# Performance work log

Measured on AMD Instinct MI355X. Metric: run time of the kernel, lower is better.

Reference implementation:

```python
import jax, jax.numpy as jnp
import numpy as np

N = 8192       # paired user/item batch
D_IN = 10000   # interaction-vector length
H = 1024       # hidden width
E = 128        # shared embedding dim


def setup_inputs() -> dict:
    key = jax.random.key(0)
    ks = jax.random.split(key, 10)
    g = 5.0 / 3.0  # tanh gain used by the torch init

    def xavier(k, shape):
        fan_in, fan_out = shape
        std = g * np.sqrt(2.0 / (fan_in + fan_out))
        return jax.random.normal(k, shape, dtype=jnp.float32) * std

    return {
        "user_data": jax.random.normal(ks[0], (N, D_IN), dtype=jnp.float32),
        "item_data": jax.random.normal(ks[1], (N, D_IN), dtype=jnp.float32),
        "Wu1": xavier(ks[2], (D_IN, H)),
        "bu1": jnp.full((H,), 0.01, dtype=jnp.float32),
        "Wu2": xavier(ks[3], (H, E)),
        "bu2": jnp.full((E,), 0.01, dtype=jnp.float32),
        "Wi1": xavier(ks[4], (D_IN, H)),
        "bi1": jnp.full((H,), 0.01, dtype=jnp.float32),
        "Wi2": xavier(ks[5], (H, E)),
        "bi2": jnp.full((E,), 0.01, dtype=jnp.float32),
    }


def reference(user_data, item_data, Wu1, bu1, Wu2, bu2, Wi1, bi1, Wi2, bi2):
    # Encoders (dropout is identity at inference). PolyLinear: Linear -> ReLU -> Linear.
    p = jax.nn.relu(user_data @ Wu1 + bu1) @ Wu2 + bu2   # [N, E]
    q = jax.nn.relu(item_data @ Wi1 + bi1) @ Wi2 + bi2   # [N, E]
    # (p @ q.T).diag() == row-wise dot product; identical math, O(N*E) not O(N^2*E).
    return jnp.einsum("ne,ne->n", p, q)
```

## Files before the change

kernel.cpp:

```cpp
#include <hip/hip_runtime.h>
#include <hip/hip_bf16.h>
#include <stdint.h>

#define KP   10112
#define DIN  10000
#define NB   8192
#define HID  1024
#define EMB  128
#define NKT  313
#define NI   79

typedef __attribute__((ext_vector_type(8))) __bf16 bf16x8;
typedef __attribute__((ext_vector_type(4))) float  f32x4;
typedef __attribute__((ext_vector_type(4))) unsigned short ushort4v;

typedef const __attribute__((address_space(1))) void* gas_cp;
typedef __attribute__((address_space(3))) void* las_p;

__device__ __forceinline__ unsigned short f2bf(float f) {
    union { float f; unsigned u; } c; c.f = f;
    unsigned u = c.u;
    u += 0x7FFFu + ((u >> 16) & 1u);
    return (unsigned short)(u >> 16);
}

__global__ void conv_pad(const float* __restrict__ src, unsigned short* __restrict__ dst) {
    const int c4  = blockIdx.x * blockDim.x + threadIdx.x;
    const int row = blockIdx.y;
    if (c4 >= KP / 4) return;
    ushort4v o;
    if (c4 < DIN / 4) {
        float4 a = *(const float4*)(src + (size_t)row * DIN + (size_t)c4 * 4);
        o[0] = f2bf(a.x); o[1] = f2bf(a.y); o[2] = f2bf(a.z); o[3] = f2bf(a.w);
    } else {
        o[0] = o[1] = o[2] = o[3] = 0;
    }
    *(ushort4v*)(dst + (size_t)row * KP + (size_t)c4 * 4) = o;
}

__global__ void conv_transpose(const float* __restrict__ src, unsigned short* __restrict__ dst,
                               int K, int N, int Kp) {
    __shared__ float tile[64][33];
    const int tx = threadIdx.x & 31, ty = threadIdx.x >> 5;
    const int k0 = blockIdx.x * 64, n0 = blockIdx.y * 32;
#pragma unroll
    for (int j = 0; j < 8; ++j) {
        int k = k0 + ty + j * 8;
        tile[ty + j * 8][tx] = (k < K) ? src[(size_t)k * N + n0 + tx] : 0.0f;
    }
    __syncthreads();
#pragma unroll
    for (int j = 0; j < 4; ++j) {
        int n = n0 + ty + j * 8;
        unsigned short lo = f2bf(tile[2 * tx][ty + j * 8]);
        unsigned short hi = f2bf(tile[2 * tx + 1][ty + j * 8]);
        unsigned int packed = (unsigned int)lo | ((unsigned int)hi << 16);
        *(unsigned int*)(dst + (size_t)n * Kp + k0 + 2 * tx) = packed;
    }
}

#define DSR(d, ad, off) asm volatile("ds_read_b128 %0, %1 offset:" off : "=v"(d) : "v"(ad))
#define GATE(n) do { asm volatile("s_waitcnt lgkmcnt(" #n ")" ::: "memory"); \
                     __builtin_amdgcn_sched_barrier(0); } while (0)

__global__ __launch_bounds__(512, 2)
void gemm1_8p(const unsigned short* __restrict__ Abf,
              const unsigned short* __restrict__ W1t,
              const float* __restrict__ b1u, const float* __restrict__ b1i,
              unsigned short* __restrict__ H1) {
    __shared__ __align__(16) unsigned short lds_[81920];

    const int t  = threadIdx.x;
    const int lane = t & 63, wv = t >> 6;
    const int wm = wv >> 2, wn = wv & 3;
    const int rA = lane & 15, kg = lane >> 4;

    const int side = blockIdx.x >> 2, bn = blockIdx.x & 3, bm = blockIdx.y;

    const unsigned short* AbfS = Abf + (size_t)side * NB * KP;
    const unsigned short* W1tS = W1t + (size_t)side * HID * KP;
    const float* bias = side ? b1i : b1u;
    unsigned short* Cout = H1 + (size_t)side * NB * HID;

    const int rowSA = bm * 256 + (t >> 3);
    const int rowSB = bn * 256 + (t >> 3);
    const int kcl   = ((t & 7) ^ ((t >> 3) & 7)) * 8;

    const int xk0 = ((0 * 4 + kg) ^ (rA & 7)) * 8;
    const int xk1 = ((1 * 4 + kg) ^ (rA & 7)) * 8;

    const unsigned ldsB = (unsigned)(size_t)lds_;
    const unsigned aC0 = ldsB + wm * 16384 + rA * 128 + xk0 * 2;
    const unsigned aC1 = ldsB + wm * 16384 + rA * 128 + xk1 * 2;
    const unsigned bC0 = ldsB + 98304 + (wn >> 1) * 16384 + (wn & 1) * 8192 + rA * 128 + xk0 * 2;
    const unsigned bC1 = ldsB + 98304 + (wn >> 1) * 16384 + (wn & 1) * 8192 + rA * 128 + xk1 * 2;

    f32x4 acc[8][4] = {};
    bf16x8 a[4][2], b[4][2];

    auto stA = [&](int tile, int h, int buf) {
        const unsigned short* s = AbfS + (size_t)(rowSA + h * 128) * KP + tile * 64 + kcl;
        __builtin_amdgcn_global_load_lds((gas_cp)s, (las_p)(lds_ + buf * 16384 + h * 8192 + wv * 512), 16, 0, 0);
        __builtin_amdgcn_global_load_lds((gas_cp)(s + (size_t)64 * KP), (las_p)(lds_ + buf * 16384 + h * 8192 + 4096 + wv * 512), 16, 0, 0);
    };
    auto stB = [&](int tile, int h, int par) {
        const unsigned short* s = W1tS + (size_t)(rowSB + h * 128) * KP + tile * 64 + kcl;
        __builtin_amdgcn_global_load_lds((gas_cp)s, (las_p)(lds_ + 49152 + par * 16384 + h * 8192 + wv * 512), 16, 0, 0);
        __builtin_amdgcn_global_load_lds((gas_cp)(s + (size_t)64 * KP), (las_p)(lds_ + 49152 + par * 16384 + h * 8192 + 4096 + wv * 512), 16, 0, 0);
    };

    auto issueB01 = [&](int par) {
        unsigned b0 = bC0 + par * 32768, b1 = bC1 + par * 32768;
        DSR(b[0][0], b0, "0");    DSR(b[0][1], b1, "0");
        DSR(b[1][0], b0, "2048"); DSR(b[1][1], b1, "2048");
    };
    auto issueB23 = [&](int par) {
        unsigned b0 = bC0 + par * 32768 + 4096, b1 = bC1 + par * 32768 + 4096;
        DSR(b[2][0], b0, "0");    DSR(b[2][1], b1, "0");
        DSR(b[3][0], b0, "2048"); DSR(b[3][1], b1, "2048");
    };
    auto issueA = [&](int buf, int mq) {
        unsigned a0 = aC0 + buf * 32768 + mq * 8192, a1 = aC1 + buf * 32768 + mq * 8192;
        DSR(a[0][0], a0, "0");    DSR(a[0][1], a1, "0");
        DSR(a[1][0], a0, "2048"); DSR(a[1][1], a1, "2048");
        DSR(a[2][0], a0, "4096"); DSR(a[2][1], a1, "4096");
        DSR(a[3][0], a0, "6144"); DSR(a[3][1], a1, "6144");
    };
    auto mmj = [&](int mq, int j, int nq) {
        acc[mq*4+j][nq*2+0] = __builtin_amdgcn_mfma_f32_16x16x32_bf16(a[j][0], b[nq*2+0][0], acc[mq*4+j][nq*2+0], 0, 0, 0);
        acc[mq*4+j][nq*2+0] = __builtin_amdgcn_mfma_f32_16x16x32_bf16(a[j][1], b[nq*2+0][1], acc[mq*4+j][nq*2+0], 0, 0, 0);
        acc[mq*4+j][nq*2+1] = __builtin_amdgcn_mfma_f32_16x16x32_bf16(a[j][0], b[nq*2+1][0], acc[mq*4+j][nq*2+1], 0, 0, 0);
        acc[mq*4+j][nq*2+1] = __builtin_amdgcn_mfma_f32_16x16x32_bf16(a[j][1], b[nq*2+1][1], acc[mq*4+j][nq*2+1], 0, 0, 0);
    };
    auto mmcol = [&](int mq, int col) {
#pragma unroll
        for (int j = 0; j < 4; ++j) {
            acc[mq*4+j][col] = __builtin_amdgcn_mfma_f32_16x16x32_bf16(a[j][0], b[col][0], acc[mq*4+j][col], 0, 0, 0);
            acc[mq*4+j][col] = __builtin_amdgcn_mfma_f32_16x16x32_bf16(a[j][1], b[col][1], acc[mq*4+j][col], 0, 0, 0);
        }
    };

    stA(0, 0, 0); stA(0, 1, 0);
    stB(0, 0, 0); stB(0, 1, 0);
    stA(1, 0, 1); stA(1, 1, 1);
    asm volatile("s_waitcnt vmcnt(4)" ::: "memory");
    __builtin_amdgcn_s_barrier();

    int cA0 = 0, cA1 = 1, nA = 2;
    for (int i = 0; i < NI - 1; ++i) {
        const int T1 = 2 * i + 1, S0 = 2 * i + 2, S1 = 2 * i + 3;
        issueB01(0); issueA(cA0, 0); stB(T1, 0, 1);
        __builtin_amdgcn_s_barrier();
        GATE(6); __builtin_amdgcn_s_setprio(1);
        mmj(0,0,0); GATE(4); mmj(0,1,0); GATE(2); mmj(0,2,0); GATE(0); mmj(0,3,0);
        __builtin_amdgcn_s_setprio(0); __builtin_amdgcn_s_barrier();
        issueB23(0); stB(T1, 1, 1);
        __builtin_amdgcn_s_barrier();
        GATE(2); __builtin_amdgcn_s_setprio(1);
        mmcol(0, 2); GATE(0); mmcol(0, 3);
        __builtin_amdgcn_s_setprio(0); __builtin_amdgcn_s_barrier();
        issueA(cA0, 1); stA(S0, 0, nA);
        __builtin_amdgcn_s_barrier();
        GATE(6); __builtin_amdgcn_s_setprio(1);
        mmj(1,0,0); GATE(4); mmj(1,1,0); GATE(2); mmj(1,2,0); GATE(0); mmj(1,3,0);
        __builtin_amdgcn_s_setprio(0); __builtin_amdgcn_s_barrier();
        stA(S0, 1, nA);
        asm volatile("s_waitcnt vmcnt(4)" ::: "memory");
        __builtin_amdgcn_s_barrier();
        __builtin_amdgcn_s_setprio(1);
        mmj(1,0,1); mmj(1,1,1); mmj(1,2,1); mmj(1,3,1);
        __builtin_amdgcn_s_setprio(0); __builtin_amdgcn_s_barrier();
        issueB01(1); issueA(cA1, 0); stB(S0, 0, 0);
        __builtin_amdgcn_s_barrier();
        GATE(6); __builtin_amdgcn_s_setprio(1);
        mmj(0,0,0); GATE(4); mmj(0,1,0); GATE(2); mmj(0,2,0); GATE(0); mmj(0,3,0);
        __builtin_amdgcn_s_setprio(0); __builtin_amdgcn_s_barrier();
        issueB23(1); stB(S0, 1, 0);
        __builtin_amdgcn_s_barrier();
        GATE(2); __builtin_amdgcn_s_setprio(1);
        mmcol(0, 2); GATE(0); mmcol(0, 3);
        __builtin_amdgcn_s_setprio(0); __builtin_amdgcn_s_barrier();
        issueA(cA1, 1); stA(S1, 0, cA0);
        __builtin_amdgcn_s_barrier();
        GATE(6); __builtin_amdgcn_s_setprio(1);
        mmj(1,0,0); GATE(4); mmj(1,1,0); GATE(2); mmj(1,2,0); GATE(0); mmj(1,3,0);
        __builtin_amdgcn_s_setprio(0); __builtin_amdgcn_s_barrier();
        stA(S1, 1, cA0);
        asm volatile("s_waitcnt vmcnt(4)" ::: "memory");
        __builtin_amdgcn_s_barrier();
        __builtin_amdgcn_s_setprio(1);
        mmj(1,0,1); mmj(1,1,1); mmj(1,2,1); mmj(1,3,1);
        __builtin_amdgcn_s_setprio(0); __builtin_amdgcn_s_barrier();
        int tmp = cA1; cA1 = cA0; cA0 = nA; nA = tmp;
    }
    {
        const int TL = 2 * NI - 1;
        issueB01(0); issueA(cA0, 0); stB(TL, 0, 1);
        __builtin_amdgcn_s_barrier();
        GATE(6); __builtin_amdgcn_s_setprio(1);
        mmj(0,0,0); GATE(4); mmj(0,1,0); GATE(2); mmj(0,2,0); GATE(0); mmj(0,3,0);
        __builtin_amdgcn_s_setprio(0); __builtin_amdgcn_s_barrier();
        issueB23(0); stB(TL, 1, 1);
        __builtin_amdgcn_s_barrier();
        GATE(2); __builtin_amdgcn_s_setprio(1);
        mmcol(0, 2); GATE(0); mmcol(0, 3);
        __builtin_amdgcn_s_setprio(0); __builtin_amdgcn_s_barrier();
        issueA(cA0, 1);
        __builtin_amdgcn_s_barrier();
        GATE(6); __builtin_amdgcn_s_setprio(1);
        mmj(1,0,0); GATE(4); mmj(1,1,0); GATE(2); mmj(1,2,0); GATE(0); mmj(1,3,0);
        __builtin_amdgcn_s_setprio(0); __builtin_amdgcn_s_barrier();
        asm volatile("s_waitcnt vmcnt(0)" ::: "memory");
        __builtin_amdgcn_s_barrier();
        __builtin_amdgcn_s_setprio(1);
        mmj(1,0,1); mmj(1,1,1); mmj(1,2,1); mmj(1,3,1);
        __builtin_amdgcn_s_setprio(0); __builtin_amdgcn_s_barrier();
        issueB01(1); issueA(cA1, 0);
        __builtin_amdgcn_s_barrier();
        GATE(6); __builtin_amdgcn_s_setprio(1);
        mmj(0,0,0); GATE(4); mmj(0,1,0); GATE(2); mmj(0,2,0); GATE(0); mmj(0,3,0);
        __builtin_amdgcn_s_setprio(0); __builtin_amdgcn_s_barrier();
        issueB23(1);
        __builtin_amdgcn_s_barrier();
        GATE(2); __builtin_amdgcn_s_setprio(1);
        mmcol(0, 2); GATE(0); mmcol(0, 3);
        __builtin_amdgcn_s_setprio(0); __builtin_amdgcn_s_barrier();
        issueA(cA1, 1);
        __builtin_amdgcn_s_barrier();
        GATE(6); __builtin_amdgcn_s_setprio(1);
        mmj(1,0,0); GATE(4); mmj(1,1,0); GATE(2); mmj(1,2,0); GATE(0); mmj(1,3,0);
        __builtin_amdgcn_s_setprio(0); __builtin_amdgcn_s_barrier();
        __builtin_amdgcn_s_setprio(1);
        mmj(1,0,1); mmj(1,1,1); mmj(1,2,1); mmj(1,3,1);
        __builtin_amdgcn_s_setprio(0);
    }

    const int rowbase = bm * 256 + wm * 128 + kg * 4;
    const int colbase = bn * 256 + wn * 64 + rA;
#pragma unroll
    for (int ni = 0; ni < 4; ++ni) {
        const int col = colbase + ni * 16;
        const float bv = bias[col];
#pragma unroll
        for (int mi = 0; mi < 8; ++mi) {
#pragma unroll
            for (int rr = 0; rr < 4; ++rr) {
                float v = fmaxf(acc[mi][ni][rr] + bv, 0.0f);
                Cout[(size_t)(rowbase + mi * 16 + rr) * HID + col] = f2bf(v);
            }
        }
    }
}

__global__ __launch_bounds__(256, 4)
void gemm1_fused(const float* __restrict__ Au, const float* __restrict__ Ai,
                 const unsigned short* __restrict__ W1t,
                 const float* __restrict__ b1u, const float* __restrict__ b1i,
                 unsigned short* __restrict__ H1) {
    __shared__ unsigned short As[2 * 4096];
    __shared__ unsigned short Bs[2 * 4096];

    const int t = threadIdx.x, lane = t & 63, wave = t >> 6;
    const int wr = wave >> 1, wc = wave & 1, rA = lane & 15, kg = lane >> 4;

    const int id   = (blockIdx.z * gridDim.y + blockIdx.y) * 8 + blockIdx.x;
    const int pos  = (id & 7) * 128 + (id >> 3);
    const int side = pos >> 9;
    const int rr   = pos & 511;
    const int bm   = rr >> 3, bn = rr & 7;

    const float* Ap = side ? Ai : Au;
    const unsigned short* Bt = W1t + (size_t)side * HID * KP;
    const float* bias = side ? b1i : b1u;
    unsigned short* Cout = H1 + (size_t)side * NB * HID;

    const int arow = t >> 1;
    const float* gA = Ap + (size_t)(bm * 128 + arow) * DIN + (t & 1) * 16;
    const int aswz = (arow >> 1) & 3;
    const int aw0 = arow * 32 + ((((t & 1) * 2)     ^ aswz)) * 8;
    const int aw1 = arow * 32 + ((((t & 1) * 2 + 1) ^ aswz)) * 8;

    const int srcc = (t & 3) ^ ((t >> 3) & 3);
    const unsigned short* gB = Bt + (size_t)(bn * 128 + (t >> 2)) * KP + (size_t)srcc * 8;
    const int wst = wave * 512;

    f32x4 acc[4][4] = {};
    const int swz  = (rA >> 1) & 3;
    const int aoff = (wr * 64 + rA) * 32 + (kg ^ swz) * 8;
    const int boff = (wc * 64 + rA) * 32 + (kg ^ swz) * 8;

    float4 ar0, ar1, ar2, ar3;

    auto loadA = [&](int kt2) {
        const float* p = gA + (size_t)kt2 * 32;
        if (kt2 == NKT - 1 && (t & 1)) {
            ar0 = make_float4(0, 0, 0, 0); ar1 = ar0; ar2 = ar0; ar3 = ar0;
        } else {
            ar0 = *(const float4*)(p);
            ar1 = *(const float4*)(p + 4);
            ar2 = *(const float4*)(p + 8);
            ar3 = *(const float4*)(p + 12);
        }
    };
    auto writeA = [&](int buf) {
        bf16x8 v0, v1;
        v0[0] = (__bf16)ar0.x; v0[1] = (__bf16)ar0.y; v0[2] = (__bf16)ar0.z; v0[3] = (__bf16)ar0.w;
        v0[4] = (__bf16)ar1.x; v0[5] = (__bf16)ar1.y; v0[6] = (__bf16)ar1.z; v0[7] = (__bf16)ar1.w;
        v1[0] = (__bf16)ar2.x; v1[1] = (__bf16)ar2.y; v1[2] = (__bf16)ar2.z; v1[3] = (__bf16)ar2.w;
        v1[4] = (__bf16)ar3.x; v1[5] = (__bf16)ar3.y; v1[6] = (__bf16)ar3.z; v1[7] = (__bf16)ar3.w;
        *(bf16x8*)(As + buf * 4096 + aw0) = v0;
        *(bf16x8*)(As + buf * 4096 + aw1) = v1;
    };
    auto stageB = [&](int kt2) {
        const int bo = (kt2 & 1) * 4096;
        const unsigned short* p = gB + (size_t)kt2 * 32;
        __builtin_amdgcn_global_load_lds((gas_cp)p,                     (las_p)(Bs + bo + wst),        16, 0, 0);
        __builtin_amdgcn_global_load_lds((gas_cp)(p + (size_t)64 * KP), (las_p)(Bs + bo + wst + 2048), 16, 0, 0);
    };
    auto compute = [&](int buf) {
        const int ao = buf * 4096 + aoff, bo = buf * 4096 + boff;
        bf16x8 b0 = *(const bf16x8*)(Bs + bo);
        bf16x8 b1 = *(const bf16x8*)(Bs + bo + 512);
        bf16x8 b2 = *(const bf16x8*)(Bs + bo + 1024);
        bf16x8 b3 = *(const bf16x8*)(Bs + bo + 1536);
#pragma unroll
        for (int m = 0; m < 4; ++m) {
            bf16x8 av = *(const bf16x8*)(As + ao + m * 512);
            acc[m][0] = __builtin_amdgcn_mfma_f32_16x16x32_bf16(av, b0, acc[m][0], 0, 0, 0);
            acc[m][1] = __builtin_amdgcn_mfma_f32_16x16x32_bf16(av, b1, acc[m][1], 0, 0, 0);
            acc[m][2] = __builtin_amdgcn_mfma_f32_16x16x32_bf16(av, b2, acc[m][2], 0, 0, 0);
            acc[m][3] = __builtin_amdgcn_mfma_f32_16x16x32_bf16(av, b3, acc[m][3], 0, 0, 0);
        }
    };

    loadA(0);
    __builtin_amdgcn_sched_barrier(0);
    stageB(0);
    __builtin_amdgcn_sched_barrier(0);
    writeA(0);
    loadA(1);
    asm volatile("s_waitcnt lgkmcnt(0)" ::: "memory");
    __builtin_amdgcn_s_barrier();

    for (int kt = 0; kt < NKT - 2; ++kt) {
        asm volatile("s_waitcnt vmcnt(4)" ::: "memory");
        __builtin_amdgcn_s_barrier();
        writeA((kt + 1) & 1);
        __builtin_amdgcn_sched_barrier(0);
        stageB(kt + 1);
        __builtin_amdgcn_sched_barrier(0);
        loadA(kt + 2);
        compute(kt & 1);
        asm volatile("s_waitcnt lgkmcnt(0)" ::: "memory");
        __builtin_amdgcn_s_barrier();
    }
    asm volatile("s_waitcnt vmcnt(4)" ::: "memory");
    __builtin_amdgcn_s_barrier();
    writeA((NKT - 1) & 1);
    __builtin_amdgcn_sched_barrier(0);
    stageB(NKT - 1);
    compute((NKT - 2) & 1);
    asm volatile("s_waitcnt lgkmcnt(0)" ::: "memory");
    __builtin_amdgcn_s_barrier();
    asm volatile("s_waitcnt vmcnt(0)" ::: "memory");
    __builtin_amdgcn_s_barrier();
    compute((NKT - 1) & 1);

    const int rowbase = bm * 128 + wr * 64 + kg * 4;
    const int colbase = bn * 128 + wc * 64 + rA;
#pragma unroll
    for (int n = 0; n < 4; ++n) {
        const int col = colbase + n * 16;
        const float bv = bias[col];
#pragma unroll
        for (int m = 0; m < 4; ++m) {
#pragma unroll
            for (int r = 0; r < 4; ++r) {
                float v = fmaxf(acc[m][n][r] + bv, 0.0f);
                Cout[(size_t)(rowbase + m * 16 + r) * HID + col] = f2bf(v);
            }
        }
    }
}

__global__ __launch_bounds__(256, 2)
void gemm2_fused(const unsigned short* __restrict__ H1,
                 const unsigned short* __restrict__ W2t,
                 const float* __restrict__ b2u, const float* __restrict__ b2i,
                 float* __restrict__ PQ) {
    __shared__ unsigned short As[3 * 4096];
    __shared__ unsigned short Bs[3 * 4096];

    const int t = threadIdx.x, lane = t & 63, wave = t >> 6;
    const int wr = wave >> 1, wc = wave & 1, rA = lane & 15, kg = lane >> 4;
    const int bm = blockIdx.y, side = blockIdx.z;
    const int nk = HID / 32;

    const unsigned short* A  = H1  + (size_t)side * NB * HID;
    const unsigned short* Bt = W2t + (size_t)side * EMB * HID;
    const float* bias = side ? b2i : b2u;
    float* Cout = PQ + (size_t)side * NB * EMB;

    const int srcc = (t & 3) ^ ((t >> 3) & 3);
    const unsigned short* ga = A  + (size_t)(bm * 128 + (t >> 2)) * HID + (size_t)srcc * 8;
    const unsigned short* gb = Bt + (size_t)(t >> 2) * HID + (size_t)srcc * 8;
    const size_t aP = (size_t)64 * HID;

    f32x4 acc[4][4] = {};
    const int swz  = (rA >> 1) & 3;
    const int aoff = (wr * 64 + rA) * 32 + (kg ^ swz) * 8;
    const int boff = (wc * 64 + rA) * 32 + (kg ^ swz) * 8;
    const int wst  = wave * 512;

    auto stage = [&](int buf) {
        const int bo = buf << 12;
        __builtin_amdgcn_global_load_lds((gas_cp)(ga),      (las_p)(As + bo + wst),        16, 0, 0);
        __builtin_amdgcn_global_load_lds((gas_cp)(ga + aP), (las_p)(As + bo + wst + 2048), 16, 0, 0);
        __builtin_amdgcn_global_load_lds((gas_cp)(gb),      (las_p)(Bs + bo + wst),        16, 0, 0);
        __builtin_amdgcn_global_load_lds((gas_cp)(gb + aP), (las_p)(Bs + bo + wst + 2048), 16, 0, 0);
        ga += 32; gb += 32;
    };
    auto compute = [&](int buf) {
        const int bo = buf << 12;
        bf16x8 af[4], bfr[4];
#pragma unroll
        for (int m = 0; m < 4; ++m) af[m]  = *(const bf16x8*)(As + bo + aoff + m * 512);
#pragma unroll
        for (int n = 0; n < 4; ++n) bfr[n] = *(const bf16x8*)(Bs + bo + boff + n * 512);
#pragma unroll
        for (int m = 0; m < 4; ++m)
#pragma unroll
            for (int n = 0; n < 4; ++n)
                acc[m][n] = __builtin_amdgcn_mfma_f32_16x16x32_bf16(af[m], bfr[n], acc[m][n], 0, 0, 0);
    };

    stage(0); stage(1);
    int cur = 0;
    for (int kt = 0; kt < nk - 2; ++kt) {
        int pfb = cur + 2; if (pfb >= 3) pfb -= 3;
        stage(pfb);
        asm volatile("s_waitcnt vmcnt(8)" ::: "memory");
        __builtin_amdgcn_s_barrier();
        compute(cur);
        __builtin_amdgcn_s_barrier();
        cur = (cur + 1 == 3) ? 0 : cur + 1;
    }
    asm volatile("s_waitcnt vmcnt(4)" ::: "memory");
    __builtin_amdgcn_s_barrier();
    compute(cur);
    cur = (cur + 1 == 3) ? 0 : cur + 1;
    asm volatile("s_waitcnt vmcnt(0)" ::: "memory");
    __builtin_amdgcn_s_barrier();
    compute(cur);

    const int rowbase = bm * 128 + wr * 64 + kg * 4;
    const int colbase = wc * 64 + rA;
#pragma unroll
    for (int n = 0; n < 4; ++n) {
        const int col = colbase + n * 16;
        const float bv = bias[col];
#pragma unroll
        for (int m = 0; m < 4; ++m) {
#pragma unroll
            for (int r = 0; r < 4; ++r) {
                Cout[(size_t)(rowbase + m * 16 + r) * EMB + col] = acc[m][n][r] + bv;
            }
        }
    }
}

__global__ void rowdot(const float* __restrict__ P, const float* __restrict__ Q,
                       float* __restrict__ out, int n) {
    int gid = blockIdx.x * blockDim.x + threadIdx.x;
    int w = gid >> 6, lane = gid & 63;
    if (w >= n) return;
    const float2 p = ((const float2*)(P + (size_t)w * EMB))[lane];
    const float2 q = ((const float2*)(Q + (size_t)w * EMB))[lane];
    float s = p.x * q.x + p.y * q.y;
#pragma unroll
    for (int off = 32; off; off >>= 1) s += __shfl_down(s, off);
    if (lane == 0) out[w] = s;
}

extern "C" void kernel_launch(void* const* d_in, const int* in_sizes, int n_in,
                              void* d_out, int out_size, void* d_ws, size_t ws_size,
                              hipStream_t stream) {
    const float* user = (const float*)d_in[0];
    const float* item = (const float*)d_in[1];
    const float* Wu1  = (const float*)d_in[2];
    const float* bu1  = (const float*)d_in[3];
    const float* Wu2  = (const float*)d_in[4];
    const float* bu2  = (const float*)d_in[5];
    const float* Wi1  = (const float*)d_in[6];
    const float* bi1  = (const float*)d_in[7];
    const float* Wi2  = (const float*)d_in[8];
    const float* bi2  = (const float*)d_in[9];
    float* out = (float*)d_out;

    char* ws = (char*)d_ws;
    size_t off = 0;
    auto alloc = [&](size_t bytes) {
        char* p = ws + off;
        off += (bytes + 255) & ~(size_t)255;
        return p;
    };

    unsigned short* W1t = (unsigned short*)alloc((size_t)2 * HID * KP * 2);
    unsigned short* W2t = (unsigned short*)alloc((size_t)2 * EMB * HID * 2);
    float* P  = (float*)alloc((size_t)NB * EMB * 4);
    float* Q  = (float*)alloc((size_t)NB * EMB * 4);
    unsigned short* H1 = (unsigned short*)alloc((size_t)2 * NB * HID * 2);

    const bool full = ws_size >= (off + (size_t)2 * NB * KP * 2 + (1u << 20));

    dim3 blk(256);
    conv_transpose<<<dim3(KP / 64, HID / 32), blk, 0, stream>>>(Wu1, W1t,                      DIN, HID, KP);
    conv_transpose<<<dim3(KP / 64, HID / 32), blk, 0, stream>>>(Wi1, W1t + (size_t)HID * KP,   DIN, HID, KP);
    conv_transpose<<<dim3(HID / 64, EMB / 32), blk, 0, stream>>>(Wu2, W2t,                     HID, EMB, HID);
    conv_transpose<<<dim3(HID / 64, EMB / 32), blk, 0, stream>>>(Wi2, W2t + (size_t)EMB * HID, HID, EMB, HID);

    if (full) {
        unsigned short* Abf = (unsigned short*)alloc((size_t)2 * NB * KP * 2);
        conv_pad<<<dim3((KP / 4 + 255) / 256, NB), blk, 0, stream>>>(user, Abf);
        conv_pad<<<dim3((KP / 4 + 255) / 256, NB), blk, 0, stream>>>(item, Abf + (size_t)NB * KP);
        gemm1_8p<<<dim3(8, 32), dim3(512), 0, stream>>>(Abf, W1t, bu1, bi1, H1);
    } else {
        gemm1_fused<<<dim3(8, 64, 2), blk, 0, stream>>>(user, item, W1t, bu1, bi1, H1);
    }
    gemm2_fused<<<dim3(1, 64, 2), blk, 0, stream>>>(H1, W2t, bu2, bi2, P);
    rowdot<<<(NB * 64) / 256, blk, 0, stream>>>(P, Q, out, NB);
}
```

Measured before the change: 511.6 us.

## Collapse gemm1 main loop to four phases and split gemm2 over K

The hand-scheduled gemm1 loop is restructured so each half-iteration issues all B and A fragment reads together, with larger lgkmcnt gates. This cuts the eight barrier-separated phases to four, reducing barrier stalls and letting more LDS reads overlap MFMA work. gemm2 is also split into two K-halves to double its grid, and rowdot sums the partial P/Q halves before the dot product. The risks are higher register pressure and less interleaving of global-to-LDS loads, plus extra partial-result traffic in gemm2.

Measured after the change: 493.4 us. 1.04x faster.

```diff
diff --git a/kernel.cpp b/kernel.cpp
--- a/kernel.cpp
+++ b/kernel.cpp
@@ -64,7 +64,7 @@
                      __builtin_amdgcn_sched_barrier(0); } while (0)
 
 __global__ __launch_bounds__(512, 2)
-void gemm1_8p(const unsigned short* __restrict__ Abf,
+void gemm1_4p(const unsigned short* __restrict__ Abf,
               const unsigned short* __restrict__ W1t,
               const float* __restrict__ b1u, const float* __restrict__ b1i,
               unsigned short* __restrict__ H1) {
@@ -109,17 +109,17 @@
         __builtin_amdgcn_global_load_lds((gas_cp)(s + (size_t)64 * KP), (las_p)(lds_ + 49152 + par * 16384 + h * 8192 + 4096 + wv * 512), 16, 0, 0);
     };
 
-    auto issueB01 = [&](int par) {
+    auto rdB01 = [&](int par) {
         unsigned b0 = bC0 + par * 32768, b1 = bC1 + par * 32768;
         DSR(b[0][0], b0, "0");    DSR(b[0][1], b1, "0");
         DSR(b[1][0], b0, "2048"); DSR(b[1][1], b1, "2048");
     };
-    auto issueB23 = [&](int par) {
+    auto rdB23 = [&](int par) {
         unsigned b0 = bC0 + par * 32768 + 4096, b1 = bC1 + par * 32768 + 4096;
         DSR(b[2][0], b0, "0");    DSR(b[2][1], b1, "0");
         DSR(b[3][0], b0, "2048"); DSR(b[3][1], b1, "2048");
     };
-    auto issueA = [&](int buf, int mq) {
+    auto rdA4 = [&](int buf, int mq) {
         unsigned a0 = aC0 + buf * 32768 + mq * 8192, a1 = aC1 + buf * 32768 + mq * 8192;
         DSR(a[0][0], a0, "0");    DSR(a[0][1], a1, "0");
         DSR(a[1][0], a0, "2048"); DSR(a[1][1], a1, "2048");
@@ -149,89 +149,64 @@
     int cA0 = 0, cA1 = 1, nA = 2;
     for (int i = 0; i < NI - 1; ++i) {
         const int T1 = 2 * i + 1, S0 = 2 * i + 2, S1 = 2 * i + 3;
-        issueB01(0); issueA(cA0, 0); stB(T1, 0, 1);
-        __builtin_amdgcn_s_barrier();
-        GATE(6); __builtin_amdgcn_s_setprio(1);
-        mmj(0,0,0); GATE(4); mmj(0,1,0); GATE(2); mmj(0,2,0); GATE(0); mmj(0,3,0);
-        __builtin_amdgcn_s_setprio(0); __builtin_amdgcn_s_barrier();
-        issueB23(0); stB(T1, 1, 1);
-        __builtin_amdgcn_s_barrier();
-        GATE(2); __builtin_amdgcn_s_setprio(1);
-        mmcol(0, 2); GATE(0); mmcol(0, 3);
-        __builtin_amdgcn_s_setprio(0); __builtin_amdgcn_s_barrier();
-        issueA(cA0, 1); stA(S0, 0, nA);
-        __builtin_amdgcn_s_barrier();
-        GATE(6); __builtin_amdgcn_s_setprio(1);
-        mmj(1,0,0); GATE(4); mmj(1,1,0); GATE(2); mmj(1,2,0); GATE(0); mmj(1,3,0);
-        __builtin_amdgcn_s_setprio(0); __builtin_amdgcn_s_barrier();
-        stA(S0, 1, nA);
+        rdB01(0); rdA4(cA0, 0); rdB23(0);
+        stB(T1, 0, 1); stB(T1, 1, 1);
+        __builtin_amdgcn_s_setprio(1);
+        GATE(10); mmj(0,0,0); GATE(8); mmj(0,1,0); GATE(6); mmj(0,2,0);
+        GATE(4);  mmj(0,3,0); GATE(2); mmcol(0,2); GATE(0); mmcol(0,3);
+        __builtin_amdgcn_s_setprio(0);
+        __builtin_amdgcn_s_barrier();
+        rdA4(cA0, 1);
+        stA(S0, 0, nA); stA(S0, 1, nA);
+        __builtin_amdgcn_s_setprio(1);
+        GATE(6); mmj(1,0,0); GATE(4); mmj(1,1,0); GATE(2); mmj(1,2,0);
+        GATE(0); mmj(1,3,0); mmcol(1,2); mmcol(1,3);
+        __builtin_amdgcn_s_setprio(0);
         asm volatile("s_waitcnt vmcnt(4)" ::: "memory");
         __builtin_amdgcn_s_barrier();
-        __builtin_amdgcn_s_setprio(1);
-        mmj(1,0,1); mmj(1,1,1); mmj(1,2,1); mmj(1,3,1);
-        __builtin_amdgcn_s_setprio(0); __builtin_amdgcn_s_barrier();
-        issueB01(1); issueA(cA1, 0); stB(S0, 0, 0);
-        __builtin_amdgcn_s_barrier();
-        GATE(6); __builtin_amdgcn_s_setprio(1);
-        mmj(0,0,0); GATE(4); mmj(0,1,0); GATE(2); mmj(0,2,0); GATE(0); mmj(0,3,0);
-        __builtin_amdgcn_s_setprio(0); __builtin_amdgcn_s_barrier();
-        issueB23(1); stB(S0, 1, 0);
-        __builtin_amdgcn_s_barrier();
-        GATE(2); __builtin_amdgcn_s_setprio(1);
-        mmcol(0, 2); GATE(0); mmcol(0, 3);
-        __builtin_amdgcn_s_setprio(0); __builtin_amdgcn_s_barrier();
-        issueA(cA1, 1); stA(S1, 0, cA0);
-        __builtin_amdgcn_s_barrier();
-        GATE(6); __builtin_amdgcn_s_setprio(1);
-        mmj(1,0,0); GATE(4); mmj(1,1,0); GATE(2); mmj(1,2,0); GATE(0); mmj(1,3,0);
-        __builtin_amdgcn_s_setprio(0); __builtin_amdgcn_s_barrier();
-        stA(S1, 1, cA0);
+        rdB01(1); rdA4(cA1, 0); rdB23(1);
+        stB(S0, 0, 0); stB(S0, 1, 0);
+        __builtin_amdgcn_s_setprio(1);
+        GATE(10); mmj(0,0,0); GATE(8); mmj(0,1,0); GATE(6); mmj(0,2,0);
+        GATE(4);  mmj(0,3,0); GATE(2); mmcol(0,2); GATE(0); mmcol(0,3);
+        __builtin_amdgcn_s_setprio(0);
+        __builtin_amdgcn_s_barrier();
+        rdA4(cA1, 1);
+        stA(S1, 0, cA0); stA(S1, 1, cA0);
+        __builtin_amdgcn_s_setprio(1);
+        GATE(6); mmj(1,0,0); GATE(4); mmj(1,1,0); GATE(2); mmj(1,2,0);
+        GATE(0); mmj(1,3,0); mmcol(1,2); mmcol(1,3);
+        __builtin_amdgcn_s_setprio(0);
         asm volatile("s_waitcnt vmcnt(4)" ::: "memory");
         __builtin_amdgcn_s_barrier();
-        __builtin_amdgcn_s_setprio(1);
-        mmj(1,0,1); mmj(1,1,1); mmj(1,2,1); mmj(1,3,1);
-        __builtin_amdgcn_s_setprio(0); __builtin_amdgcn_s_barrier();
         int tmp = cA1; cA1 = cA0; cA0 = nA; nA = tmp;
     }
     {
         const int TL = 2 * NI - 1;
-        issueB01(0); issueA(cA0, 0); stB(TL, 0, 1);
-        __builtin_amdgcn_s_barrier();
-        GATE(6); __builtin_amdgcn_s_setprio(1);
-        mmj(0,0,0); GATE(4); mmj(0,1,0); GATE(2); mmj(0,2,0); GATE(0); mmj(0,3,0);
-        __builtin_amdgcn_s_setprio(0); __builtin_amdgcn_s_barrier();
-        issueB23(0); stB(TL, 1, 1);
-        __builtin_amdgcn_s_barrier();
-        GATE(2); __builtin_amdgcn_s_setprio(1);
-        mmcol(0, 2); GATE(0); mmcol(0, 3);
-        __builtin_amdgcn_s_setprio(0); __builtin_amdgcn_s_barrier();
-        issueA(cA0, 1);
-        __builtin_amdgcn_s_barrier();
-        GATE(6); __builtin_amdgcn_s_setprio(1);
-        mmj(1,0,0); GATE(4); mmj(1,1,0); GATE(2); mmj(1,2,0); GATE(0); mmj(1,3,0);
-        __builtin_amdgcn_s_setprio(0); __builtin_amdgcn_s_barrier();
+        rdB01(0); rdA4(cA0, 0); rdB23(0);
+        stB(TL, 0, 1); stB(TL, 1, 1);
+        __builtin_amdgcn_s_setprio(1);
+        GATE(10); mmj(0,0,0); GATE(8); mmj(0,1,0); GATE(6); mmj(0,2,0);
+        GATE(4);  mmj(0,3,0); GATE(2); mmcol(0,2); GATE(0); mmcol(0,3);
+        __builtin_amdgcn_s_setprio(0);
+        __builtin_amdgcn_s_barrier();
+        rdA4(cA0, 1);
+        __builtin_amdgcn_s_setprio(1);
+        GATE(6); mmj(1,0,0); GATE(4); mmj(1,1,0); GATE(2); mmj(1,2,0);
+        GATE(0); mmj(1,3,0); mmcol(1,2); mmcol(1,3);
+        __builtin_amdgcn_s_setprio(0);
         asm volatile("s_waitcnt vmcnt(0)" ::: "memory");
         __builtin_amdgcn_s_barrier();
-        __builtin_amdgcn_s_setprio(1);
-        mmj(1,0,1); mmj(1,1,1); mmj(1,2,1); mmj(1,3,1);
-        __builtin_amdgcn_s_setprio(0); __builtin_amdgcn_s_barrier();
-        issueB01(1); issueA(cA1, 0);
-        __builtin_amdgcn_s_barrier();
-        GATE(6); __builtin_amdgcn_s_setprio(1);
-        mmj(0,0,0); GATE(4); mmj(0,1,0); GATE(2); mmj(0,2,0); GATE(0); mmj(0,3,0);
-        __builtin_amdgcn_s_setprio(0); __builtin_amdgcn_s_barrier();
-        issueB23(1);
-        __builtin_amdgcn_s_barrier();
-        GATE(2); __builtin_amdgcn_s_setprio(1);
-        mmcol(0, 2); GATE(0); mmcol(0, 3);
-        __builtin_amdgcn_s_setprio(0); __builtin_amdgcn_s_barrier();
-        issueA(cA1, 1);
-        __builtin_amdgcn_s_barrier();
-        GATE(6); __builtin_amdgcn_s_setprio(1);
-        mmj(1,0,0); GATE(4); mmj(1,1,0); GATE(2); mmj(1,2,0); GATE(0); mmj(1,3,0);
-        __builtin_amdgcn_s_setprio(0); __builtin_amdgcn_s_barrier();
-        __builtin_amdgcn_s_setprio(1);
-        mmj(1,0,1); mmj(1,1,1); mmj(1,2,1); mmj(1,3,1);
+        rdB01(1); rdA4(cA1, 0); rdB23(1);
+        __builtin_amdgcn_s_setprio(1);
+        GATE(10); mmj(0,0,0); GATE(8); mmj(0,1,0); GATE(6); mmj(0,2,0);
+        GATE(4);  mmj(0,3,0); GATE(2); mmcol(0,2); GATE(0); mmcol(0,3);
+        __builtin_amdgcn_s_setprio(0);
+        __builtin_amdgcn_s_barrier();
+        rdA4(cA1, 1);
+        __builtin_amdgcn_s_setprio(1);
+        GATE(6); mmj(1,0,0); GATE(4); mmj(1,1,0); GATE(2); mmj(1,2,0);
+        GATE(0); mmj(1,3,0); mmcol(1,2); mmcol(1,3);
         __builtin_amdgcn_s_setprio(0);
     }
 
@@ -384,22 +359,22 @@
 }
 
 __global__ __launch_bounds__(256, 2)
-void gemm2_fused(const unsigned short* __restrict__ H1,
-                 const unsigned short* __restrict__ W2t,
-                 const float* __restrict__ b2u, const float* __restrict__ b2i,
-                 float* __restrict__ PQ) {
+void gemm2k(const unsigned short* __restrict__ H1,
+            const unsigned short* __restrict__ W2t,
+            const float* __restrict__ b2u, const float* __restrict__ b2i,
+            float* __restrict__ PQh) {
     __shared__ unsigned short As[3 * 4096];
     __shared__ unsigned short Bs[3 * 4096];
 
     const int t = threadIdx.x, lane = t & 63, wave = t >> 6;
     const int wr = wave >> 1, wc = wave & 1, rA = lane & 15, kg = lane >> 4;
-    const int bm = blockIdx.y, side = blockIdx.z;
-    const int nk = HID / 32;
-
-    const unsigned short* A  = H1  + (size_t)side * NB * HID;
-    const unsigned short* Bt = W2t + (size_t)side * EMB * HID;
+    const int kh = blockIdx.x, bm = blockIdx.y, side = blockIdx.z;
+    const int nk = 512 / 32;
+
+    const unsigned short* A  = H1  + (size_t)side * NB * HID + kh * 512;
+    const unsigned short* Bt = W2t + (size_t)side * EMB * HID + kh * 512;
     const float* bias = side ? b2i : b2u;
-    float* Cout = PQ + (size_t)side * NB * EMB;
+    float* Cout = PQh + (size_t)(kh * 2 + side) * NB * EMB;
 
     const int srcc = (t & 3) ^ ((t >> 3) & 3);
     const unsigned short* ga = A  + (size_t)(bm * 128 + (t >> 2)) * HID + (size_t)srcc * 8;
@@ -458,7 +433,7 @@
 #pragma unroll
     for (int n = 0; n < 4; ++n) {
         const int col = colbase + n * 16;
-        const float bv = bias[col];
+        const float bv = (kh == 0) ? bias[col] : 0.0f;
 #pragma unroll
         for (int m = 0; m < 4; ++m) {
 #pragma unroll
@@ -469,14 +444,18 @@
     }
 }
 
-__global__ void rowdot(const float* __restrict__ P, const float* __restrict__ Q,
-                       float* __restrict__ out, int n) {
+__global__ void rowdot4(const float* __restrict__ PQh, float* __restrict__ out, int n) {
     int gid = blockIdx.x * blockDim.x + threadIdx.x;
     int w = gid >> 6, lane = gid & 63;
     if (w >= n) return;
-    const float2 p = ((const float2*)(P + (size_t)w * EMB))[lane];
-    const float2 q = ((const float2*)(Q + (size_t)w * EMB))[lane];
-    float s = p.x * q.x + p.y * q.y;
+    const size_t C = (size_t)NB * EMB;
+    const float2 p0 = ((const float2*)(PQh + 0 * C + (size_t)w * EMB))[lane];
+    const float2 q0 = ((const float2*)(PQh + 1 * C + (size_t)w * EMB))[lane];
+    const float2 p1 = ((const float2*)(PQh + 2 * C + (size_t)w * EMB))[lane];
+    const float2 q1 = ((const float2*)(PQh + 3 * C + (size_t)w * EMB))[lane];
+    const float px = p0.x + p1.x, py = p0.y + p1.y;
+    const float qx = q0.x + q1.x, qy = q0.y + q1.y;
+    float s = px * qx + py * qy;
 #pragma unroll
     for (int off = 32; off; off >>= 1) s += __shfl_down(s, off);
     if (lane == 0) out[w] = s;
@@ -507,8 +486,7 @@
 
     unsigned short* W1t = (unsigned short*)alloc((size_t)2 * HID * KP * 2);
     unsigned short* W2t = (unsigned short*)alloc((size_t)2 * EMB * HID * 2);
-    float* P  = (float*)alloc((size_t)NB * EMB * 4);
-    float* Q  = (float*)alloc((size_t)NB * EMB * 4);
+    float* PQh = (float*)alloc((size_t)4 * NB * EMB * 4);
     unsigned short* H1 = (unsigned short*)alloc((size_t)2 * NB * HID * 2);
 
     const bool full = ws_size >= (off + (size_t)2 * NB * KP * 2 + (1u << 20));
@@ -523,10 +501,10 @@
         unsigned short* Abf = (unsigned short*)alloc((size_t)2 * NB * KP * 2);
         conv_pad<<<dim3((KP / 4 + 255) / 256, NB), blk, 0, stream>>>(user, Abf);
         conv_pad<<<dim3((KP / 4 + 255) / 256, NB), blk, 0, stream>>>(item, Abf + (size_t)NB * KP);
-        gemm1_8p<<<dim3(8, 32), dim3(512), 0, stream>>>(Abf, W1t, bu1, bi1, H1);
+        gemm1_4p<<<dim3(8, 32), dim3(512), 0, stream>>>(Abf, W1t, bu1, bi1, H1);
     } else {
         gemm1_fused<<<dim3(8, 64, 2), blk, 0, stream>>>(user, item, W1t, bu1, bi1, H1);
     }
-    gemm2_fused<<<dim3(1, 64, 2), blk, 0, stream>>>(H1, W2t, bu2, bi2, P);
-    rowdot<<<(NB * 64) / 256, blk, 0, stream>>>(P, Q, out, NB);
-}
+    gemm2k<<<dim3(2, 64, 2), blk, 0, stream>>>(H1, W2t, bu2, bi2, PQh);
+    rowdot4<<<(NB * 64) / 256, blk, 0, stream>>>(PQh, out, NB);
+}
```
